# Optimization experiments

Measured on AMD Instinct MI355X. Metric: run time of the kernel, lower is better.

Reference implementation:

```python
import jax, jax.numpy as jnp
import numpy as np

N_CODES = 4096
D = 256


def setup_inputs() -> dict:
    key = jax.random.key(0)
    k_v, k_w = jax.random.split(key)
    v = jax.random.normal(k_v, (8, 2048, D), dtype=jnp.float32)
    # Embedding init ~ N(0,1), then softmax over dim=1, then row 0 set to 1/d (empty feature)
    w = jax.random.normal(k_w, (N_CODES, D), dtype=jnp.float32)
    w = jax.nn.softmax(w, axis=1)
    w = w.at[0].set(1.0 / D)
    return {"v": v, "vectors": w}


def reference(v, vectors):
    n, d = vectors.shape
    cb = vectors[1:]  # exclude the fixed empty feature at index 0
    # ||v - c||^2 = ||v||^2 - 2 v.c + ||c||^2  (avoids [..., n, d] intermediate)
    v2 = jnp.sum(v * v, axis=-1, keepdims=True)              # [..., 1]
    c2 = jnp.sum(cb * cb, axis=-1)                           # [n-1]
    diff = v2 - 2.0 * jnp.einsum('...d,nd->...n', v, cb) + c2  # [..., n-1]
    idx = jnp.argmin(diff, axis=-1) + 1                      # [...]
    # empty-feature mask: any component differs from 1/d
    mask = jnp.any(v != (1.0 / d), axis=-1)
    idx = jnp.where(mask, idx, 0)
    out = vectors[idx]                                       # gather == onehot @ vectors
    loss = jnp.mean(jnp.square(out - jax.lax.stop_gradient(v)))
    used = jnp.array(0, dtype=jnp.int32)  # eval mode: usage pool is empty
    return out, idx, loss, used
```

## Files before the change

### kernel.cpp

```cpp
#include <hip/hip_runtime.h>
#include <hip/hip_fp16.h>
#include <math.h>
#include <stdint.h>


#define M_TOTAL 16384
#define NCODES  4096
#define D_DIM   256

#define OUT_OFF_IDX  (M_TOTAL * D_DIM)
#define OUT_OFF_LOSS (OUT_OFF_IDX + M_TOTAL)

#define VPLANE (M_TOTAL * D_DIM)

typedef _Float16 half8 __attribute__((ext_vector_type(8)));
typedef float    float16v __attribute__((ext_vector_type(16)));

__global__ __launch_bounds__(256) void prep_kernel(
    const float* __restrict__ V, const float* __restrict__ W,
    _Float16* __restrict__ Vhi, _Float16* __restrict__ Vlo,
    _Float16* __restrict__ Bp, float* __restrict__ v2, float* __restrict__ c2,
    uint64_t* __restrict__ pk)
{
  __shared__ float T[16 * 264];
  const int t = threadIdx.x;
  const int rloc = t >> 4, seg = t & 15;
  const bool isW = blockIdx.x < 256;
  const int bid2 = isW ? blockIdx.x : (blockIdx.x - 256);
  const int row = bid2 * 16 + rloc;
  const float* X = isW ? W : V;

  if (!isW && bid2 < 64) pk[bid2 * 256 + t] = ~0ULL;

  const float* src = X + (size_t)row * D_DIM + seg * 16;
  float4 x[4];
#pragma unroll
  for (int u = 0; u < 4; ++u) x[u] = ((const float4*)src)[u];
  union { half8 v; _Float16 e[8]; } uh[2], ul[2];
#pragma unroll
  for (int u = 0; u < 4; ++u) {
    float e4[4] = {x[u].x, x[u].y, x[u].z, x[u].w};
#pragma unroll
    for (int j = 0; j < 4; ++j) {
      const int e = u * 4 + j;
      float s = e4[j] * 1024.0f;
      _Float16 h = (_Float16)s;
      uh[e >> 3].e[e & 7] = h;
      ul[e >> 3].e[e & 7] = (_Float16)(s - (float)h);
    }
    *(float4*)&T[rloc * 264 + seg * 16 + u * 4] = x[u];
  }
  if (isW) {
    const int panel = row >> 5, nin = row & 31;
    _Float16* dst = Bp + ((size_t)panel * 16 + seg) * 2048 + nin * 8;
#pragma unroll
    for (int lh = 0; lh < 2; ++lh) {
      *(half8*)(dst + lh * 256)        = uh[lh].v;
      *(half8*)(dst + 1024 + lh * 256) = ul[lh].v;
    }
  } else {
    _Float16* hd = Vhi + (size_t)row * D_DIM + seg * 16;
    _Float16* ld = Vlo + (size_t)row * D_DIM + seg * 16;
    *(half8*)hd = uh[0].v; *(half8*)(hd + 8) = uh[1].v;
    *(half8*)ld = ul[0].v; *(half8*)(ld + 8) = ul[1].v;
  }
  __syncthreads();
  const int half = (t >> 3) & 1, j = t & 7;
  const float* tr = &T[rloc * 264 + half * 128 + j];
  float r = __fmul_rn(tr[0], tr[0]);
#pragma unroll
  for (int i = 1; i < 16; ++i) { float e = tr[8 * i]; r = __fadd_rn(r, __fmul_rn(e, e)); }
  r = __fadd_rn(r, __shfl_xor(r, 1));
  r = __fadd_rn(r, __shfl_xor(r, 2));
  r = __fadd_rn(r, __shfl_xor(r, 4));
  r = __fadd_rn(r, __shfl_xor(r, 8));
  if ((t & 15) == 0) { if (isW) c2[row] = r; else v2[row] = r; }
}

__global__ __launch_bounds__(256, 2) void vq_mfma_kernel(
    const _Float16* __restrict__ Vhi, const _Float16* __restrict__ Vlo,
    const _Float16* __restrict__ Bp,
    const float* __restrict__ v2, const float* __restrict__ c2,
    uint64_t* __restrict__ pk)
{
  __shared__ __align__(16) char smem_raw[69632];
  _Float16* As = (_Float16*)smem_raw;
  uint64_t* red2 = (uint64_t*)(smem_raw + 65536);

  const int tid  = threadIdx.x;
  const int lane = tid & 63;
  const int wave = tid >> 6;
  const int wr = wave >> 1, wc = wave & 1;
  const int l31 = lane & 31, lhi = lane >> 5;

  const int bid = blockIdx.x;
  const int panel = (bid & 7) * 4 + ((bid >> 3) & 3);
  const int mblk  = bid >> 5;
  const int m0 = mblk * 256;
  const int n0 = panel * 128;
  const int p32 = panel * 4 + wc * 2;

  int src[4], dst[4];
#pragma unroll
  for (int u = 0; u < 4; ++u) {
    const int g = tid + 256 * u, m = g >> 2, kb = g & 3;
    src[u] = (m0 + m) * D_DIM + kb * 8;
    dst[u] = m * 32 + (kb ^ (m & 3)) * 8;
  }

  float16v acc[4][2];
#pragma unroll
  for (int mb = 0; mb < 4; ++mb)
#pragma unroll
    for (int nb = 0; nb < 2; ++nb) acc[mb][nb] = (float16v)0.0f;

  half8 sh[4], sl[4];
#pragma unroll
  for (int u = 0; u < 4; ++u) {
    sh[u] = *(const half8*)(Vhi + src[u]);
    sl[u] = *(const half8*)(Vlo + src[u]);
  }
#pragma unroll
  for (int u = 0; u < 4; ++u) {
    *(half8*)(As + dst[u])        = sh[u];
    *(half8*)(As + 8192 + dst[u]) = sl[u];
  }

  half8 bh[2][2], bl[2][2];
#pragma unroll
  for (int nb = 0; nb < 2; ++nb) {
    const _Float16* bp = Bp + ((size_t)(p32 + nb) * 16) * 2048 + lane * 8;
    bh[0][nb] = *(const half8*)bp;
    bl[0][nb] = *(const half8*)(bp + 1024);
  }
  __syncthreads();

  for (int kt = 0; kt < 8; ++kt) {
    const int cur = kt & 1;
    _Float16* Ac = As + cur * 16384;
    if (kt < 7) {
#pragma unroll
      for (int u = 0; u < 4; ++u) {
        sh[u] = *(const half8*)(Vhi + src[u] + (kt + 1) * 32);
        sl[u] = *(const half8*)(Vlo + src[u] + (kt + 1) * 32);
      }
    }
#pragma unroll
    for (int ks = 0; ks < 2; ++ks) {
      const int kstep = kt * 2 + ks;
      const int pcur = kstep & 1, pnxt = pcur ^ 1;
      if (kstep < 15) {
#pragma unroll
        for (int nb = 0; nb < 2; ++nb) {
          const _Float16* bp = Bp + ((size_t)(p32 + nb) * 16 + kstep + 1) * 2048 + lane * 8;
          bh[pnxt][nb] = *(const half8*)bp;
          bl[pnxt][nb] = *(const half8*)(bp + 1024);
        }
      }
      half8 ah[4], al[4];
#pragma unroll
      for (int mb = 0; mb < 4; ++mb) {
        const int m = wr * 128 + mb * 32 + l31;
        const int c = (ks * 2 + lhi) ^ (m & 3);
        ah[mb] = *(const half8*)(Ac + m * 32 + c * 8);
        al[mb] = *(const half8*)(Ac + 8192 + m * 32 + c * 8);
      }
#pragma unroll
      for (int nb = 0; nb < 2; ++nb)
#pragma unroll
        for (int mb = 0; mb < 4; ++mb)
          acc[mb][nb] = __builtin_amdgcn_mfma_f32_32x32x16_f16(ah[mb], bh[pcur][nb], acc[mb][nb], 0, 0, 0);
#pragma unroll
      for (int nb = 0; nb < 2; ++nb)
#pragma unroll
        for (int mb = 0; mb < 4; ++mb)
          acc[mb][nb] = __builtin_amdgcn_mfma_f32_32x32x16_f16(ah[mb], bl[pcur][nb], acc[mb][nb], 0, 0, 0);
#pragma unroll
      for (int nb = 0; nb < 2; ++nb)
#pragma unroll
        for (int mb = 0; mb < 4; ++mb)
          acc[mb][nb] = __builtin_amdgcn_mfma_f32_32x32x16_f16(al[mb], bh[pcur][nb], acc[mb][nb], 0, 0, 0);
    }
    if (kt < 7) {
      _Float16* An = As + (cur ^ 1) * 16384;
#pragma unroll
      for (int u = 0; u < 4; ++u) {
        *(half8*)(An + dst[u])        = sh[u];
        *(half8*)(An + 8192 + dst[u]) = sl[u];
      }
    }
    __syncthreads();
  }

  float c2r[2];
#pragma unroll
  for (int nb = 0; nb < 2; ++nb) c2r[nb] = c2[n0 + wc * 64 + nb * 32 + l31];

  uint64_t* wbuf = (uint64_t*)smem_raw + wave * 1056;

#pragma unroll
  for (int mb = 0; mb < 4; ++mb) {
#pragma unroll
    for (int r = 0; r < 16; ++r) {
      const int rowin = (r & 3) + 8 * (r >> 2) + 4 * lhi;
      const float v2m = v2[m0 + wr * 128 + mb * 32 + rowin];
      uint64_t b = ~0ULL;
#pragma unroll
      for (int nb = 0; nb < 2; ++nb) {
        const int n = n0 + wc * 64 + nb * 32 + l31;
        float dot = acc[mb][nb][r] * 0x1p-20f;
        float dd  = __fadd_rn(__fsub_rn(v2m, 2.0f * dot), c2r[nb]);
        if (n == 0) dd = INFINITY;
        uint64_t p = ((uint64_t)__float_as_uint(dd) << 32) | (uint32_t)n;
        if (p < b) b = p;
      }
      wbuf[(r * 2 + lhi) * 33 + l31] = b;
    }
    __syncthreads();
    {
      const int f = lane >> 1, hf = lane & 1;
      const uint64_t* rp = wbuf + f * 33 + hf * 16;
      uint64_t m = rp[0];
#pragma unroll
      for (int i = 1; i < 16; ++i) { uint64_t v = rp[i]; if (v < m) m = v; }
      uint64_t o = __shfl_xor((unsigned long long)m, 1);
      if (o < m) m = o;
      if (hf == 0) {
        const int r_ = f >> 1, lh2 = f & 1;
        const int rowin = (r_ & 3) + 8 * (r_ >> 2) + 4 * lh2;
        red2[(wr * 128 + mb * 32 + rowin) * 2 + wc] = m;
      }
    }
    __syncthreads();
  }

  uint64_t a0 = red2[tid * 2], a1 = red2[tid * 2 + 1];
  atomicMin((unsigned long long*)&pk[m0 + tid], (unsigned long long)(a0 < a1 ? a0 : a1));
}

__global__ __launch_bounds__(256) void gather_kernel(
    const float* __restrict__ V, const float* __restrict__ W,
    const uint64_t* __restrict__ pk,
    float* __restrict__ out, float* __restrict__ outIdx,
    float* __restrict__ lossPartial)
{
  const int q = blockIdx.x * 4 + (threadIdx.x >> 6);
  const int l = threadIdx.x & 63;
  const uint64_t b = pk[q];
  float4 vv = *(const float4*)(V + (size_t)q * D_DIM + l * 4);
  const float inv = 0.00390625f;
  bool ne = (vv.x != inv) | (vv.y != inv) | (vv.z != inv) | (vv.w != inv);
  const int idx = __ballot(ne) ? (int)(uint32_t)b : 0;
  float4 o4 = *(const float4*)(W + (size_t)idx * D_DIM + l * 4);
  *(float4*)(out + (size_t)q * D_DIM + l * 4) = o4;
  if (l == 0) outIdx[q] = (float)idx;
  float dx = o4.x - vv.x, dy = o4.y - vv.y, dz = o4.z - vv.z, dw = o4.w - vv.w;
  float s = dx * dx + dy * dy + dz * dz + dw * dw;
#pragma unroll
  for (int off = 32; off; off >>= 1) s += __shfl_xor(s, off);
  if (l == 0) lossPartial[q] = s;
}

__global__ __launch_bounds__(256) void finalize_kernel(
    const float* __restrict__ lossPartial, float* __restrict__ out)
{
  const int t = threadIdx.x;
  __shared__ float red[256];
  float s = 0.0f;
  for (int i = t; i < M_TOTAL; i += 256) s += lossPartial[i];
  red[t] = s;
  __syncthreads();
  for (int st = 128; st > 0; st >>= 1) {
    if (t < st) red[t] += red[t + st];
    __syncthreads();
  }
  if (t == 0) {
    out[0] = (float)((double)red[0] / (double)(M_TOTAL * D_DIM));
    out[1] = 0.0f;
  }
}

extern "C" void kernel_launch(void* const* d_in, const int* in_sizes, int n_in,
                              void* d_out, int out_size, void* d_ws, size_t ws_size,
                              hipStream_t stream) {
  const float* V = (const float*)d_in[0];
  const float* W = (const float*)d_in[1];
  float* out = (float*)d_out;

  _Float16* Vhi = (_Float16*)d_out;
  _Float16* Vlo = Vhi + VPLANE;

  char* ws = (char*)d_ws;
  _Float16* Bp  = (_Float16*)(ws);
  float*    c2  = (float*)(ws + 8388608);
  float*    v2  = (float*)(ws + 8388608 + 16384);
  uint64_t* pk  = (uint64_t*)(ws + 8388608 + 16384 + 65536);
  float* lossPartial = (float*)(ws + 8388608 + 16384 + 65536 + 131072);

  prep_kernel<<<1280, 256, 0, stream>>>(V, W, Vhi, Vlo, Bp, v2, c2, pk);
  vq_mfma_kernel<<<2048, 256, 0, stream>>>(Vhi, Vlo, Bp, v2, c2, pk);
  gather_kernel<<<M_TOTAL / 4, 256, 0, stream>>>(V, W, pk, out, out + OUT_OFF_IDX, lossPartial);
  finalize_kernel<<<1, 256, 0, stream>>>(lossPartial, out + OUT_OFF_LOSS);
}
```

Before: 210.1 us.

## Pre-pack V into MFMA fragment layout and load A directly from global

The prep kernel now writes the hi/lo fp16 split of V in the same panel-packed, per-lane fragment order already used for the codebook. The MFMA kernel then loads A operands straight from global memory into registers, with register double-buffering. This removes the LDS staging, the swizzled shared-memory writes and reads, and the per-k-tile __syncthreads, and shrinks the shared-memory footprint. In exchange, each wave fetches its own A fragments from global/L2 instead of sharing one LDS copy across the two waves in a row, which increases global load traffic and register pressure.

```diff
diff --git a/kernel.cpp b/kernel.cpp
--- a/kernel.cpp
+++ b/kernel.cpp
@@ -11,15 +11,13 @@
 #define OUT_OFF_IDX  (M_TOTAL * D_DIM)
 #define OUT_OFF_LOSS (OUT_OFF_IDX + M_TOTAL)
 
-#define VPLANE (M_TOTAL * D_DIM)
-
 typedef _Float16 half8 __attribute__((ext_vector_type(8)));
 typedef float    float16v __attribute__((ext_vector_type(16)));
 
 __global__ __launch_bounds__(256) void prep_kernel(
     const float* __restrict__ V, const float* __restrict__ W,
-    _Float16* __restrict__ Vhi, _Float16* __restrict__ Vlo,
-    _Float16* __restrict__ Bp, float* __restrict__ v2, float* __restrict__ c2,
+    _Float16* __restrict__ Vp, _Float16* __restrict__ Bp,
+    float* __restrict__ v2, float* __restrict__ c2,
     uint64_t* __restrict__ pk)
 {
   __shared__ float T[16 * 264];
@@ -59,10 +57,12 @@
       *(half8*)(dst + 1024 + lh * 256) = ul[lh].v;
     }
   } else {
-    _Float16* hd = Vhi + (size_t)row * D_DIM + seg * 16;
-    _Float16* ld = Vlo + (size_t)row * D_DIM + seg * 16;
-    *(half8*)hd = uh[0].v; *(half8*)(hd + 8) = uh[1].v;
-    *(half8*)ld = ul[0].v; *(half8*)(ld + 8) = ul[1].v;
+    _Float16* dst = Vp + ((size_t)(row >> 5) * 16 + seg) * 1024 + (row & 31) * 8;
+#pragma unroll
+    for (int lh = 0; lh < 2; ++lh) {
+      *(half8*)(dst + lh * 256)        = uh[lh].v;
+      *(half8*)(dst + 512 + lh * 256)  = ul[lh].v;
+    }
   }
   __syncthreads();
   const int half = (t >> 3) & 1, j = t & 7;
@@ -78,14 +78,12 @@
 }
 
 __global__ __launch_bounds__(256, 2) void vq_mfma_kernel(
-    const _Float16* __restrict__ Vhi, const _Float16* __restrict__ Vlo,
-    const _Float16* __restrict__ Bp,
+    const _Float16* __restrict__ Vp, const _Float16* __restrict__ Bp,
     const float* __restrict__ v2, const float* __restrict__ c2,
     uint64_t* __restrict__ pk)
 {
-  __shared__ __align__(16) char smem_raw[69632];
-  _Float16* As = (_Float16*)smem_raw;
-  uint64_t* red2 = (uint64_t*)(smem_raw + 65536);
+  __shared__ __align__(16) char smem_raw[37888];
+  uint64_t* red2 = (uint64_t*)(smem_raw + 33792);
 
   const int tid  = threadIdx.x;
   const int lane = tid & 63;
@@ -99,14 +97,16 @@
   const int m0 = mblk * 256;
   const int n0 = panel * 128;
   const int p32 = panel * 4 + wc * 2;
-
-  int src[4], dst[4];
-#pragma unroll
-  for (int u = 0; u < 4; ++u) {
-    const int g = tid + 256 * u, m = g >> 2, kb = g & 3;
-    src[u] = (m0 + m) * D_DIM + kb * 8;
-    dst[u] = m * 32 + (kb ^ (m & 3)) * 8;
-  }
+  const int mp0 = mblk * 8 + wr * 4;
+
+  const _Float16* pA[4];
+#pragma unroll
+  for (int mb = 0; mb < 4; ++mb)
+    pA[mb] = Vp + ((size_t)(mp0 + mb) * 16) * 1024 + lane * 8;
+  const _Float16* pB[2];
+#pragma unroll
+  for (int nb = 0; nb < 2; ++nb)
+    pB[nb] = Bp + ((size_t)(p32 + nb) * 16) * 2048 + lane * 8;
 
   float16v acc[4][2];
 #pragma unroll
@@ -114,82 +114,51 @@
 #pragma unroll
     for (int nb = 0; nb < 2; ++nb) acc[mb][nb] = (float16v)0.0f;
 
-  half8 sh[4], sl[4];
-#pragma unroll
-  for (int u = 0; u < 4; ++u) {
-    sh[u] = *(const half8*)(Vhi + src[u]);
-    sl[u] = *(const half8*)(Vlo + src[u]);
-  }
-#pragma unroll
-  for (int u = 0; u < 4; ++u) {
-    *(half8*)(As + dst[u])        = sh[u];
-    *(half8*)(As + 8192 + dst[u]) = sl[u];
-  }
-
-  half8 bh[2][2], bl[2][2];
+  half8 ah[2][4], al[2][4], bh[2][2], bl[2][2];
+#pragma unroll
+  for (int mb = 0; mb < 4; ++mb) {
+    ah[0][mb] = *(const half8*)(pA[mb]);
+    al[0][mb] = *(const half8*)(pA[mb] + 512);
+  }
 #pragma unroll
   for (int nb = 0; nb < 2; ++nb) {
-    const _Float16* bp = Bp + ((size_t)(p32 + nb) * 16) * 2048 + lane * 8;
-    bh[0][nb] = *(const half8*)bp;
-    bl[0][nb] = *(const half8*)(bp + 1024);
-  }
-  __syncthreads();
-
-  for (int kt = 0; kt < 8; ++kt) {
-    const int cur = kt & 1;
-    _Float16* Ac = As + cur * 16384;
-    if (kt < 7) {
-#pragma unroll
-      for (int u = 0; u < 4; ++u) {
-        sh[u] = *(const half8*)(Vhi + src[u] + (kt + 1) * 32);
-        sl[u] = *(const half8*)(Vlo + src[u] + (kt + 1) * 32);
-      }
-    }
-#pragma unroll
-    for (int ks = 0; ks < 2; ++ks) {
-      const int kstep = kt * 2 + ks;
-      const int pcur = kstep & 1, pnxt = pcur ^ 1;
-      if (kstep < 15) {
-#pragma unroll
-        for (int nb = 0; nb < 2; ++nb) {
-          const _Float16* bp = Bp + ((size_t)(p32 + nb) * 16 + kstep + 1) * 2048 + lane * 8;
-          bh[pnxt][nb] = *(const half8*)bp;
-          bl[pnxt][nb] = *(const half8*)(bp + 1024);
-        }
-      }
-      half8 ah[4], al[4];
+    bh[0][nb] = *(const half8*)(pB[nb]);
+    bl[0][nb] = *(const half8*)(pB[nb] + 1024);
+  }
+
+#pragma unroll
+  for (int kstep = 0; kstep < 16; ++kstep) {
+    const int cur = kstep & 1, nxt = cur ^ 1;
+    if (kstep < 15) {
+      const int ko = kstep + 1;
 #pragma unroll
       for (int mb = 0; mb < 4; ++mb) {
-        const int m = wr * 128 + mb * 32 + l31;
-        const int c = (ks * 2 + lhi) ^ (m & 3);
-        ah[mb] = *(const half8*)(Ac + m * 32 + c * 8);
-        al[mb] = *(const half8*)(Ac + 8192 + m * 32 + c * 8);
-      }
-#pragma unroll
-      for (int nb = 0; nb < 2; ++nb)
-#pragma unroll
-        for (int mb = 0; mb < 4; ++mb)
-          acc[mb][nb] = __builtin_amdgcn_mfma_f32_32x32x16_f16(ah[mb], bh[pcur][nb], acc[mb][nb], 0, 0, 0);
-#pragma unroll
-      for (int nb = 0; nb < 2; ++nb)
-#pragma unroll
-        for (int mb = 0; mb < 4; ++mb)
-          acc[mb][nb] = __builtin_amdgcn_mfma_f32_32x32x16_f16(ah[mb], bl[pcur][nb], acc[mb][nb], 0, 0, 0);
-#pragma unroll
-      for (int nb = 0; nb < 2; ++nb)
-#pragma unroll
-        for (int mb = 0; mb < 4; ++mb)
-          acc[mb][nb] = __builtin_amdgcn_mfma_f32_32x32x16_f16(al[mb], bh[pcur][nb], acc[mb][nb], 0, 0, 0);
-    }
-    if (kt < 7) {
-      _Float16* An = As + (cur ^ 1) * 16384;
-#pragma unroll
-      for (int u = 0; u < 4; ++u) {
-        *(half8*)(An + dst[u])        = sh[u];
-        *(half8*)(An + 8192 + dst[u]) = sl[u];
-      }
-    }
-    __syncthreads();
+        const _Float16* p = pA[mb] + ko * 1024;
+        ah[nxt][mb] = *(const half8*)p;
+        al[nxt][mb] = *(const half8*)(p + 512);
+      }
+#pragma unroll
+      for (int nb = 0; nb < 2; ++nb) {
+        const _Float16* p = pB[nb] + ko * 2048;
+        bh[nxt][nb] = *(const half8*)p;
+        bl[nxt][nb] = *(const half8*)(p + 1024);
+      }
+    }
+#pragma unroll
+    for (int nb = 0; nb < 2; ++nb)
+#pragma unroll
+      for (int mb = 0; mb < 4; ++mb)
+        acc[mb][nb] = __builtin_amdgcn_mfma_f32_32x32x16_f16(ah[cur][mb], bh[cur][nb], acc[mb][nb], 0, 0, 0);
+#pragma unroll
+    for (int nb = 0; nb < 2; ++nb)
+#pragma unroll
+      for (int mb = 0; mb < 4; ++mb)
+        acc[mb][nb] = __builtin_amdgcn_mfma_f32_32x32x16_f16(ah[cur][mb], bl[cur][nb], acc[mb][nb], 0, 0, 0);
+#pragma unroll
+    for (int nb = 0; nb < 2; ++nb)
+#pragma unroll
+      for (int mb = 0; mb < 4; ++mb)
+        acc[mb][nb] = __builtin_amdgcn_mfma_f32_32x32x16_f16(al[cur][mb], bh[cur][nb], acc[mb][nb], 0, 0, 0);
   }
 
   float c2r[2];
@@ -287,8 +256,7 @@
   const float* W = (const float*)d_in[1];
   float* out = (float*)d_out;
 
-  _Float16* Vhi = (_Float16*)d_out;
-  _Float16* Vlo = Vhi + VPLANE;
+  _Float16* Vp = (_Float16*)d_out;
 
   char* ws = (char*)d_ws;
   _Float16* Bp  = (_Float16*)(ws);
@@ -297,8 +265,8 @@
   uint64_t* pk  = (uint64_t*)(ws + 8388608 + 16384 + 65536);
   float* lossPartial = (float*)(ws + 8388608 + 16384 + 65536 + 131072);
 
-  prep_kernel<<<1280, 256, 0, stream>>>(V, W, Vhi, Vlo, Bp, v2, c2, pk);
-  vq_mfma_kernel<<<2048, 256, 0, stream>>>(Vhi, Vlo, Bp, v2, c2, pk);
+  prep_kernel<<<1280, 256, 0, stream>>>(V, W, Vp, Bp, v2, c2, pk);
+  vq_mfma_kernel<<<2048, 256, 0, stream>>>(Vp, Bp, v2, c2, pk);
   gather_kernel<<<M_TOTAL / 4, 256, 0, stream>>>(V, W, pk, out, out + OUT_OFF_IDX, lossPartial);
   finalize_kernel<<<1, 256, 0, stream>>>(lossPartial, out + OUT_OFF_LOSS);
 }
```

Result: faster. 198.8 us (-5.3%).
